# Kernel optimization log

Measured on AMD Instinct MI355X. Metric: run time of the kernel, lower is better.

## Reference

```python
import jax, jax.numpy as jnp
import numpy as np

CONF_THRES = 0.25
IOU_THRES = 0.45
MAX_DET = 300
MAX_WH = 4096.0  # class offset for class-aware (non-agnostic) NMS
B, N, NC = 16, 25200, 80


def setup_inputs() -> dict:
    key = jax.random.key(0)
    k1, k2 = jax.random.split(key)
    p = jax.random.uniform(k1, (B, N, 5 + NC), dtype=jnp.float32)
    # scale to realistic YOLO pixel-space xywh for a 640x640 image
    cx = p[..., 0] * 640.0
    cy = p[..., 1] * 640.0
    w = p[..., 2] * 96.0 + 4.0
    h = p[..., 3] * 96.0 + 4.0
    obj = p[..., 4]
    cls = p[..., 5:] * 0.9
    prediction = jnp.concatenate([jnp.stack([cx, cy, w, h, obj], axis=-1), cls], axis=-1)
    logits = jax.random.normal(k2, (B, N, NC), dtype=jnp.float32)
    return {"prediction": prediction, "logits": logits}


def xywh2xyxy(b):
    cx, cy, w, h = b[..., 0], b[..., 1], b[..., 2], b[..., 3]
    return jnp.stack([cx - w * 0.5, cy - h * 0.5, cx + w * 0.5, cy + h * 0.5], axis=-1)


def _iou_one_vs_all(box, boxes):
    # box: [4], boxes: [N,4] in xyxy
    lt = jnp.maximum(box[:2], boxes[:, :2])
    rb = jnp.minimum(box[2:], boxes[:, 2:])
    wh = jnp.clip(rb - lt, 0.0)
    inter = wh[:, 0] * wh[:, 1]
    a1 = (box[2] - box[0]) * (box[3] - box[1])
    a2 = (boxes[:, 2] - boxes[:, 0]) * (boxes[:, 3] - boxes[:, 1])
    return inter / (a1 + a2 - inter + 1e-9)


def _nms_image(x6, boxes_off, scores, log_):
    # greedy NMS, fixed MAX_DET iterations; suppressed/invalid scores are -1
    def step(s, _):
        best = jnp.argmax(s)
        keep = s[best] > 0.0
        iou = _iou_one_vs_all(boxes_off[best], boxes_off)
        s = jnp.where(iou > IOU_THRES, -1.0, s)  # also suppresses 'best' (IoU=1)
        return s, (best, keep)
    _, (idx, keep) = jax.lax.scan(step, scores, None, length=MAX_DET)
    km = keep.astype(x6.dtype)[:, None]
    dets = x6[idx] * km          # [MAX_DET, 6] zero-padded
    lg = log_[idx] * km          # [MAX_DET, 80]
    return dets, lg, keep


def reference(prediction, logits):
    obj = prediction[..., 4]                          # [B,N]
    cls_conf = prediction[..., 5:] * obj[..., None]   # x[:,5:] *= x[:,4:5]
    conf = jnp.max(cls_conf, axis=-1)                 # best class conf
    j = jnp.argmax(cls_conf, axis=-1)                 # best class index
    box = xywh2xyxy(prediction[..., :4])              # [B,N,4]
    valid = (obj > CONF_THRES) & (conf > CONF_THRES)
    scores = jnp.where(valid, conf, -1.0)
    boxes_off = box + (j.astype(box.dtype) * MAX_WH)[..., None]  # class-aware offset
    x6 = jnp.concatenate([box, conf[..., None], j.astype(box.dtype)[..., None]], axis=-1)
    dets, lg, keep = jax.vmap(_nms_image)(x6, boxes_off, scores, logits)
    return dets, lg, keep
```

## Files before the change

kernel.cpp:

```cpp
#include <hip/hip_runtime.h>
#include <cstdint>

#define BB 16
#define NN 25200
#define NCLS 80
#define ROW 85
#define MAXDET 300
#define HBINS 2048
#define CAP2 512
#define TGT 448
#define CONF_T 0.25f
#define IOU_T 0.45f
#define NT 1024

static const size_t OFF_KEYS  = 1612800;
static const size_t OFF_CBOX  = OFF_KEYS  + 65536;
static const size_t OFF_RAW   = OFF_CBOX  + 131072;
static const size_t OFF_CCLS  = OFF_RAW   + 131072;
static const size_t OFF_CCNT  = OFF_CCLS  + 32768;
static const size_t OFF_MASK  = OFF_CCNT  + 64;
static const size_t OFF_MASKT = OFF_MASK  + 524288;

__global__ __launch_bounds__(256) void k_pre(const float* __restrict__ pred,
                                             float* __restrict__ scoreArr) {
    int tid = threadIdx.x;
    int t = tid & 3;
    int row = blockIdx.x * 64 + (tid >> 2);
    const float* rp = pred + (size_t)row * ROW;
    int start = (t == 0) ? 0 : (1 + 21 * t);
    int cnt   = (t == 0) ? 22 : 21;
    float obj = rp[4];
    float best = -1.0f; int bc = 1 << 20;
#pragma unroll
    for (int k = 0; k < 22; ++k) {
        if (k < cnt) {
            int col = start + k;
            if (col >= 5) {
                float v = __fmul_rn(rp[col], obj);
                if (v > best) { best = v; bc = col; }
            }
        }
    }
#pragma unroll
    for (int d = 1; d <= 2; d <<= 1) {
        float ob = __shfl_xor(best, d);
        int   oc = __shfl_xor(bc, d);
        if (ob > best || (ob == best && oc < bc)) { best = ob; bc = oc; }
    }
    if (t == 0) {
        bool valid = (obj > CONF_T) && (best > CONF_T);
        scoreArr[row] = valid ? best : -1.0f;
    }
}

__global__ __launch_bounds__(NT) void k_sel(const float* __restrict__ pred,
                                            const float* __restrict__ scoreArr,
                                            unsigned long long* __restrict__ keysG,
                                            float4* __restrict__ cboxG,
                                            float4* __restrict__ rawG,
                                            unsigned* __restrict__ cclsG,
                                            int* __restrict__ ccnt) {
    __shared__ unsigned hist[HBINS];
    __shared__ unsigned csum[257];
    __shared__ unsigned long long keys[CAP2];
    __shared__ int flags[2];

    int b = blockIdx.x, tid = threadIdx.x;
    int lane = tid & 63;

    for (int k = tid; k < HBINS; k += NT) hist[k] = 0u;
    if (tid == 0) { flags[0] = 0; flags[1] = 0; }
    __syncthreads();

    float sreg[25];
#pragma unroll
    for (int t = 0; t < 25; ++t) {
        int n = tid + t * NT;
        float s = (n < NN) ? scoreArr[(size_t)b * NN + n] : -1.0f;
        sreg[t] = s;
        if (s > 0.0f) {
            unsigned key = (__float_as_uint(s) - 0x3E800000u) >> 13;
            if (key > HBINS - 1) key = HBINS - 1;
            atomicAdd(&hist[key], 1u);
        }
    }
    __syncthreads();

    if (tid < 256) {
        unsigned cs = 0;
#pragma unroll
        for (int t = 0; t < 8; ++t) cs += hist[tid * 8 + t];
        csum[tid] = cs;
    }
    __syncthreads();
    for (int off = 1; off < 256; off <<= 1) {
        unsigned v = 0, add = 0;
        if (tid < 256) {
            v = csum[tid];
            add = (tid + off < 256) ? csum[tid + off] : 0u;
        }
        __syncthreads();
        if (tid < 256) csum[tid] = v + add;
        __syncthreads();
    }
    if (tid < 256) {
        unsigned Sc = csum[tid];
        unsigned Sn = (tid < 255) ? csum[tid + 1] : 0u;
        if (Sc >= TGT && (tid == 255 || Sn < TGT)) {
            unsigned cum = Sn;
            int t = tid * 8;
            for (int k = tid * 8 + 7; k >= tid * 8; --k) {
                cum += hist[k];
                if (cum >= TGT) { t = k; break; }
            }
            flags[1] = t;
        }
    }
    __syncthreads();
    unsigned thr = (unsigned)flags[1];

#pragma unroll
    for (int t = 0; t < 25; ++t) {
        int n = tid + t * NT;
        float s = sreg[t];
        bool win = false;
        if (s > 0.0f) {
            unsigned key = (__float_as_uint(s) - 0x3E800000u) >> 13;
            if (key > HBINS - 1) key = HBINS - 1;
            win = (key >= thr);
        }
        unsigned long long m = __ballot(win);
        if (m) {
            int lead = __ffsll((long long)m) - 1;
            int base = 0;
            if (lane == lead) base = atomicAdd(&flags[0], __popcll(m));
            base = __shfl(base, lead);
            if (win) {
                int pos = base + __popcll(m & ((1ULL << lane) - 1ULL));
                if (pos < CAP2)
                    keys[pos] = ((unsigned long long)__float_as_uint(s) << 32)
                              | (unsigned long long)(0xFFFFFFFFu - (unsigned)n);
            }
        }
    }
    __syncthreads();
    int c = min(flags[0], CAP2);
    for (int p = tid; p < CAP2; p += NT)
        if (p >= c) keys[p] = 0ULL;
    __syncthreads();

    for (int k = 2; k <= CAP2; k <<= 1) {
        for (int j = k >> 1; j > 0; j >>= 1) {
            for (int i = tid; i < CAP2; i += NT) {
                int ixj = i ^ j;
                if (ixj > i) {
                    unsigned long long k1 = keys[i], k2 = keys[ixj];
                    bool sw = ((i & k) == 0) ? (k1 < k2) : (k1 > k2);
                    if (sw) { keys[i] = k2; keys[ixj] = k1; }
                }
            }
            __syncthreads();
        }
    }

    if (tid < CAP2) {
        int p = tid;
        if (p < c) {
            int n = (int)(0xFFFFFFFFu - (unsigned)keys[p]);
            const float* rp = pred + ((size_t)b * NN + n) * ROW;
            float cx = rp[0], cy = rp[1], w = rp[2], h = rp[3], obj = rp[4];
            float best = __fmul_rn(rp[5], obj);
            int bj = 0;
#pragma unroll 8
            for (int cc = 1; cc < NCLS; ++cc) {
                float v = __fmul_rn(rp[5 + cc], obj);
                if (v > best) { best = v; bj = cc; }
            }
            float hw = __fmul_rn(w, 0.5f), hh = __fmul_rn(h, 0.5f);
            float4 bb = make_float4(__fsub_rn(cx, hw), __fsub_rn(cy, hh),
                                    __fadd_rn(cx, hw), __fadd_rn(cy, hh));
            rawG[b * CAP2 + p] = bb;
            float off = __fmul_rn((float)bj, 4096.0f);
            cboxG[b * CAP2 + p] = make_float4(__fadd_rn(bb.x, off), __fadd_rn(bb.y, off),
                                              __fadd_rn(bb.z, off), __fadd_rn(bb.w, off));
            cclsG[b * CAP2 + p] = (unsigned)bj;
        } else {
            rawG[b * CAP2 + p]  = make_float4(0.f, 0.f, 0.f, 0.f);
            cboxG[b * CAP2 + p] = make_float4(0.f, 0.f, 0.f, 0.f);
            cclsG[b * CAP2 + p] = 0u;
        }
        keysG[b * CAP2 + p] = keys[p];
    }
    if (tid == 0) ccnt[b] = c;
}

__global__ __launch_bounds__(256) void k_mask(const float4* __restrict__ cboxG,
                                              const int* __restrict__ ccnt,
                                              unsigned long long* __restrict__ maskG,
                                              unsigned long long* __restrict__ maskTG) {
    __shared__ float4 cb[CAP2];
    int b = blockIdx.x >> 3, w = blockIdx.x & 7;
    int tid = threadIdx.x;
    cb[tid] = cboxG[b * CAP2 + tid];
    cb[256 + tid] = cboxG[b * CAP2 + 256 + tid];
    __syncthreads();
    int c = min(ccnt[b], CAP2);
    int jbase = w << 6;
    for (int i = tid; i < CAP2; i += 256) {
        unsigned long long m = 0ULL;
        if (i < c && i < jbase + 63) {
            float4 ci = cb[i];
            float a1 = __fmul_rn(__fsub_rn(ci.z, ci.x), __fsub_rn(ci.w, ci.y));
#pragma unroll 4
            for (int jj = 0; jj < 64; ++jj) {
                int j = jbase + jj;
                float4 cj = cb[j];
                float ltx = fmaxf(ci.x, cj.x), lty = fmaxf(ci.y, cj.y);
                float rbx = fminf(ci.z, cj.z), rby = fminf(ci.w, cj.w);
                float ww = fmaxf(__fsub_rn(rbx, ltx), 0.0f);
                float hh = fmaxf(__fsub_rn(rby, lty), 0.0f);
                float inter = __fmul_rn(ww, hh);
                if (j > i && inter > 0.0f) {
                    float a2 = __fmul_rn(__fsub_rn(cj.z, cj.x), __fsub_rn(cj.w, cj.y));
                    float denom = __fadd_rn(__fsub_rn(__fadd_rn(a1, a2), inter), 1e-9f);
                    if (inter / denom > IOU_T) m |= (1ULL << jj);
                }
            }
        }
        maskG[((size_t)(b * CAP2 + i)) * 8 + w] = m;
    }
    if (tid < 64) {
        int l = tid, p = jbase + l;
        unsigned long long m = 0ULL;
        if (p < c) {
            float4 cl = cb[p];
            float a2 = __fmul_rn(__fsub_rn(cl.z, cl.x), __fsub_rn(cl.w, cl.y));
            for (int ii = 0; ii < 64; ++ii) {
                float4 ci = cb[jbase + ii];
                float ltx = fmaxf(ci.x, cl.x), lty = fmaxf(ci.y, cl.y);
                float rbx = fminf(ci.z, cl.z), rby = fminf(ci.w, cl.w);
                float ww = fmaxf(__fsub_rn(rbx, ltx), 0.0f);
                float hh = fmaxf(__fsub_rn(rby, lty), 0.0f);
                float inter = __fmul_rn(ww, hh);
                if (ii < l && inter > 0.0f) {
                    float a1 = __fmul_rn(__fsub_rn(ci.z, ci.x), __fsub_rn(ci.w, ci.y));
                    float denom = __fadd_rn(__fsub_rn(__fadd_rn(a1, a2), inter), 1e-9f);
                    if (inter / denom > IOU_T) m |= (1ULL << ii);
                }
            }
        }
        maskTG[((size_t)(b * 8 + w)) * 64 + l] = m;
    }
}

__global__ __launch_bounds__(NT) void k_fin(const float* __restrict__ logits,
                                            const unsigned long long* __restrict__ keysG,
                                            const float4* __restrict__ rawG,
                                            const unsigned* __restrict__ cclsG,
                                            const int* __restrict__ ccnt,
                                            const unsigned long long* __restrict__ maskG,
                                            const unsigned long long* __restrict__ maskTG,
                                            float* __restrict__ out) {
    __shared__ unsigned long long keepm_s[8];
    __shared__ unsigned kidx[64];
    __shared__ unsigned rowsrc_s[MAXDET];
    __shared__ int s_kept;

    int b = blockIdx.x, tid = threadIdx.x;
    int c = min(ccnt[b], CAP2);

    if (tid < 64) {
        int lane = tid;
        unsigned long long remq = 0ULL;
        int kept = 0;
        for (int w = 0; w < 8; ++w) {
            int base = w << 6;
            unsigned long long tw = __shfl(remq, w);
            bool pre = ((tw >> lane) & 1ULL) != 0ULL;
            bool validl = (base + lane) < c;
            unsigned long long Cl = maskTG[((size_t)(b * 8 + w)) * 64 + lane];
            unsigned long long initK = __ballot(validl && !pre);
            unsigned long long K = initK;
            for (int it = 0; it < 64; ++it) {
                bool sup = (Cl & K & ((1ULL << lane) - 1ULL)) != 0ULL;
                unsigned long long K2 = initK & __ballot(!sup);
                if (K2 == K) break;
                K = K2;
            }
            int limit = MAXDET - kept;
            int nk = __popcll(K);
            if (nk > limit) {
                if (limit <= 0) K = 0ULL;
                else {
                    int pref = __popcll(K & ((2ULL << lane) - 1ULL));
                    bool el = ((K >> lane) & 1ULL) && (pref <= limit);
                    K = __ballot(el);
                }
            }
            kept += __popcll(K);
            if (lane == 0) keepm_s[w] = K;
            if (K != 0ULL && w < 7) {
                if ((K >> lane) & 1ULL) {
                    int r = __popcll(K & ((1ULL << lane) - 1ULL));
                    kidx[r] = (unsigned)lane;
                }
                __builtin_amdgcn_s_waitcnt(0);
                int nkk = __popcll(K);
                int q = lane & 7, slot = lane >> 3;
                unsigned long long acc = 0ULL;
                for (int t = slot; t < nkk; t += 8)
                    acc |= maskG[((size_t)(b * CAP2 + base + (int)kidx[t])) * 8 + q];
                acc |= __shfl_xor(acc, 8);
                acc |= __shfl_xor(acc, 16);
                acc |= __shfl_xor(acc, 32);
                if (slot == 0) remq |= acc;
            }
        }
        if (lane == 0) s_kept = kept;
    }
    __syncthreads();
    int kept = s_kept;

    float* dets = out;
    float* lg   = out + (size_t)BB * MAXDET * 6;
    float* kpo  = lg  + (size_t)BB * MAXDET * NCLS;

    for (int p = tid; p < CAP2; p += NT) {
        if (p < c) {
            int w = p >> 6, bitp = p & 63;
            unsigned long long kw = keepm_s[w];
            if ((kw >> bitp) & 1ULL) {
                int rank = __popcll(kw & ((1ULL << bitp) - 1ULL));
                for (int q = 0; q < w; ++q) rank += __popcll(keepm_s[q]);
                if (rank < MAXDET) {
                    float4 bb = rawG[b * CAP2 + p];
                    unsigned long long key = keysG[b * CAP2 + p];
                    float* dr = dets + ((size_t)b * MAXDET + rank) * 6;
                    dr[0] = bb.x; dr[1] = bb.y; dr[2] = bb.z; dr[3] = bb.w;
                    dr[4] = __uint_as_float((unsigned)(key >> 32));
                    dr[5] = (float)cclsG[b * CAP2 + p];
                    rowsrc_s[rank] = 0xFFFFFFFFu - (unsigned)key;
                }
            }
        }
    }
    for (int i = tid; i < MAXDET; i += NT) {
        if (i >= kept) {
            float* dr = dets + ((size_t)b * MAXDET + i) * 6;
#pragma unroll
            for (int q = 0; q < 6; ++q) dr[q] = 0.0f;
        }
        kpo[b * MAXDET + i] = (i < kept) ? 1.0f : 0.0f;
    }
    __syncthreads();
    for (int i = tid; i < MAXDET * NCLS; i += NT) {
        int t = i / NCLS, col = i - t * NCLS;
        float v = 0.0f;
        if (t < kept) v = logits[((size_t)b * NN + rowsrc_s[t]) * NCLS + col];
        lg[(size_t)b * MAXDET * NCLS + i] = v;
    }
}

extern "C" void kernel_launch(void* const* d_in, const int* in_sizes, int n_in,
                              void* d_out, int out_size, void* d_ws, size_t ws_size,
                              hipStream_t stream) {
    const float* pred   = (const float*)d_in[0];
    const float* logits = (const float*)d_in[1];
    float* out = (float*)d_out;
    char* ws = (char*)d_ws;

    float* scr = (float*)ws;
    unsigned long long* keysG  = (unsigned long long*)(ws + OFF_KEYS);
    float4* cboxG              = (float4*)(ws + OFF_CBOX);
    float4* rawG               = (float4*)(ws + OFF_RAW);
    unsigned* cclsG            = (unsigned*)(ws + OFF_CCLS);
    int* ccnt                  = (int*)(ws + OFF_CCNT);
    unsigned long long* maskG  = (unsigned long long*)(ws + OFF_MASK);
    unsigned long long* maskTG = (unsigned long long*)(ws + OFF_MASKT);

    k_pre<<<6300, 256, 0, stream>>>(pred, scr);
    k_sel<<<BB, NT, 0, stream>>>(pred, scr, keysG, cboxG, rawG, cclsG, ccnt);
    k_mask<<<BB * 8, 256, 0, stream>>>(cboxG, ccnt, maskG, maskTG);
    k_fin<<<BB, NT, 0, stream>>>(logits, keysG, rawG, cclsG, ccnt, maskG, maskTG, out);
}
```

Baseline: 346.9 us.

## Fuse histogram into pre-pass, split selection, merge mask and NMS into one kernel

Per-image score histograms are now built in k_pre with global atomics, so k_sel no longer rebuilds them. k_sel is split into 8 slices per image so compaction runs across more blocks. Sorting, box gathering, IoU mask building and greedy NMS move into a single k_fin kernel that keeps keys, boxes and masks in shared memory, which removes the separate k_mask launch and its global round trips. The cost is a memset, heavy global atomic traffic on the histogram, and a large shared-memory footprint in k_fin, where only 16 blocks do all the mask work.

New measurement: 388.0 us. +11.8%, slower.

```diff
diff --git a/kernel.cpp b/kernel.cpp
--- a/kernel.cpp
+++ b/kernel.cpp
@@ -11,18 +11,14 @@
 #define TGT 448
 #define CONF_T 0.25f
 #define IOU_T 0.45f
-#define NT 1024
-
-static const size_t OFF_KEYS  = 1612800;
-static const size_t OFF_CBOX  = OFF_KEYS  + 65536;
-static const size_t OFF_RAW   = OFF_CBOX  + 131072;
-static const size_t OFF_CCLS  = OFF_RAW   + 131072;
-static const size_t OFF_CCNT  = OFF_CCLS  + 32768;
-static const size_t OFF_MASK  = OFF_CCNT  + 64;
-static const size_t OFF_MASKT = OFF_MASK  + 524288;
+
+static const size_t OFF_CNT  = 131072;
+static const size_t OFF_KEYS = 131136;
+static const size_t OFF_SCR  = 196672;
 
 __global__ __launch_bounds__(256) void k_pre(const float* __restrict__ pred,
-                                             float* __restrict__ scoreArr) {
+                                             float* __restrict__ scoreArr,
+                                             unsigned* __restrict__ hist) {
     int tid = threadIdx.x;
     int t = tid & 3;
     int row = blockIdx.x * 64 + (tid >> 2);
@@ -50,79 +46,61 @@
     if (t == 0) {
         bool valid = (obj > CONF_T) && (best > CONF_T);
         scoreArr[row] = valid ? best : -1.0f;
+        if (valid) {
+            unsigned key = (__float_as_uint(best) - 0x3E800000u) >> 13;
+            if (key > HBINS - 1) key = HBINS - 1;
+            atomicAdd(&hist[(row / NN) * HBINS + key], 1u);
+        }
     }
 }
 
-__global__ __launch_bounds__(NT) void k_sel(const float* __restrict__ pred,
-                                            const float* __restrict__ scoreArr,
-                                            unsigned long long* __restrict__ keysG,
-                                            float4* __restrict__ cboxG,
-                                            float4* __restrict__ rawG,
-                                            unsigned* __restrict__ cclsG,
-                                            int* __restrict__ ccnt) {
-    __shared__ unsigned hist[HBINS];
+__global__ __launch_bounds__(256) void k_sel(const float* __restrict__ scoreArr,
+                                             const unsigned* __restrict__ histG,
+                                             int* __restrict__ cntG,
+                                             unsigned long long* __restrict__ keysG) {
+    __shared__ unsigned h[HBINS];
     __shared__ unsigned csum[257];
-    __shared__ unsigned long long keys[CAP2];
-    __shared__ int flags[2];
-
-    int b = blockIdx.x, tid = threadIdx.x;
-    int lane = tid & 63;
-
-    for (int k = tid; k < HBINS; k += NT) hist[k] = 0u;
-    if (tid == 0) { flags[0] = 0; flags[1] = 0; }
-    __syncthreads();
-
-    float sreg[25];
+    __shared__ int s_thr;
+    int b = blockIdx.x >> 3, slice = blockIdx.x & 7;
+    int tid = threadIdx.x, lane = tid & 63;
+
+    for (int k = tid; k < HBINS; k += 256) h[k] = histG[b * HBINS + k];
+    if (tid == 0) s_thr = 0;
+    __syncthreads();
+
+    unsigned cs = 0;
 #pragma unroll
-    for (int t = 0; t < 25; ++t) {
-        int n = tid + t * NT;
-        float s = (n < NN) ? scoreArr[(size_t)b * NN + n] : -1.0f;
-        sreg[t] = s;
-        if (s > 0.0f) {
-            unsigned key = (__float_as_uint(s) - 0x3E800000u) >> 13;
-            if (key > HBINS - 1) key = HBINS - 1;
-            atomicAdd(&hist[key], 1u);
-        }
-    }
-    __syncthreads();
-
-    if (tid < 256) {
-        unsigned cs = 0;
-#pragma unroll
-        for (int t = 0; t < 8; ++t) cs += hist[tid * 8 + t];
-        csum[tid] = cs;
-    }
+    for (int t = 0; t < 8; ++t) cs += h[tid * 8 + t];
+    csum[tid] = cs;
     __syncthreads();
     for (int off = 1; off < 256; off <<= 1) {
-        unsigned v = 0, add = 0;
-        if (tid < 256) {
-            v = csum[tid];
-            add = (tid + off < 256) ? csum[tid + off] : 0u;
-        }
+        unsigned v = csum[tid];
+        unsigned add = (tid + off < 256) ? csum[tid + off] : 0u;
         __syncthreads();
-        if (tid < 256) csum[tid] = v + add;
+        csum[tid] = v + add;
         __syncthreads();
     }
-    if (tid < 256) {
+    {
         unsigned Sc = csum[tid];
         unsigned Sn = (tid < 255) ? csum[tid + 1] : 0u;
         if (Sc >= TGT && (tid == 255 || Sn < TGT)) {
             unsigned cum = Sn;
             int t = tid * 8;
             for (int k = tid * 8 + 7; k >= tid * 8; --k) {
-                cum += hist[k];
+                cum += h[k];
                 if (cum >= TGT) { t = k; break; }
             }
-            flags[1] = t;
-        }
-    }
-    __syncthreads();
-    unsigned thr = (unsigned)flags[1];
-
-#pragma unroll
-    for (int t = 0; t < 25; ++t) {
-        int n = tid + t * NT;
-        float s = sreg[t];
+            s_thr = t;
+        }
+    }
+    __syncthreads();
+    unsigned thr = (unsigned)s_thr;
+
+    int base_n = slice * (NN / 8);
+    for (int r = 0; r < 13; ++r) {
+        int n = base_n + r * 256 + tid;
+        bool in = (r * 256 + tid) < (NN / 8);
+        float s = in ? scoreArr[(size_t)b * NN + n] : -1.0f;
         bool win = false;
         if (s > 0.0f) {
             unsigned key = (__float_as_uint(s) - 0x3E800000u) >> 13;
@@ -132,27 +110,45 @@
         unsigned long long m = __ballot(win);
         if (m) {
             int lead = __ffsll((long long)m) - 1;
-            int base = 0;
-            if (lane == lead) base = atomicAdd(&flags[0], __popcll(m));
-            base = __shfl(base, lead);
+            int basep = 0;
+            if (lane == lead) basep = atomicAdd(&cntG[b], __popcll(m));
+            basep = __shfl(basep, lead);
             if (win) {
-                int pos = base + __popcll(m & ((1ULL << lane) - 1ULL));
+                int pos = basep + __popcll(m & ((1ULL << lane) - 1ULL));
                 if (pos < CAP2)
-                    keys[pos] = ((unsigned long long)__float_as_uint(s) << 32)
-                              | (unsigned long long)(0xFFFFFFFFu - (unsigned)n);
-            }
-        }
-    }
-    __syncthreads();
-    int c = min(flags[0], CAP2);
-    for (int p = tid; p < CAP2; p += NT)
-        if (p >= c) keys[p] = 0ULL;
+                    keysG[b * CAP2 + pos] = ((unsigned long long)__float_as_uint(s) << 32)
+                                          | (unsigned long long)(0xFFFFFFFFu - (unsigned)n);
+            }
+        }
+    }
+}
+
+__global__ __launch_bounds__(1024) void k_fin(const float* __restrict__ pred,
+                                              const float* __restrict__ logits,
+                                              const unsigned long long* __restrict__ keysG,
+                                              const int* __restrict__ ccnt,
+                                              float* __restrict__ out) {
+    __shared__ unsigned long long keys[CAP2];
+    __shared__ float4 cbox[CAP2];
+    __shared__ float4 rawb[CAP2];
+    __shared__ unsigned ccls[CAP2];
+    __shared__ unsigned long long maskS[CAP2 * 8];
+    __shared__ unsigned long long maskT[8 * 64];
+    __shared__ unsigned rowsrc_s[MAXDET];
+    __shared__ unsigned kidx[64];
+    __shared__ unsigned long long keepm_s[8];
+    __shared__ int s_kept;
+
+    int b = blockIdx.x, tid = threadIdx.x;
+    int c = min(ccnt[b], CAP2);
+
+    if (tid < CAP2) keys[tid] = (tid < c) ? keysG[b * CAP2 + tid] : 0ULL;
     __syncthreads();
 
     for (int k = 2; k <= CAP2; k <<= 1) {
         for (int j = k >> 1; j > 0; j >>= 1) {
-            for (int i = tid; i < CAP2; i += NT) {
-                int ixj = i ^ j;
+            if (tid < CAP2) {
+                int i = tid, ixj = i ^ j;
                 if (ixj > i) {
                     unsigned long long k1 = keys[i], k2 = keys[ixj];
                     bool sw = ((i & k) == 0) ? (k1 < k2) : (k1 > k2);
@@ -179,42 +175,31 @@
             float hw = __fmul_rn(w, 0.5f), hh = __fmul_rn(h, 0.5f);
             float4 bb = make_float4(__fsub_rn(cx, hw), __fsub_rn(cy, hh),
                                     __fadd_rn(cx, hw), __fadd_rn(cy, hh));
-            rawG[b * CAP2 + p] = bb;
+            rawb[p] = bb;
             float off = __fmul_rn((float)bj, 4096.0f);
-            cboxG[b * CAP2 + p] = make_float4(__fadd_rn(bb.x, off), __fadd_rn(bb.y, off),
-                                              __fadd_rn(bb.z, off), __fadd_rn(bb.w, off));
-            cclsG[b * CAP2 + p] = (unsigned)bj;
+            cbox[p] = make_float4(__fadd_rn(bb.x, off), __fadd_rn(bb.y, off),
+                                  __fadd_rn(bb.z, off), __fadd_rn(bb.w, off));
+            ccls[p] = (unsigned)bj;
         } else {
-            rawG[b * CAP2 + p]  = make_float4(0.f, 0.f, 0.f, 0.f);
-            cboxG[b * CAP2 + p] = make_float4(0.f, 0.f, 0.f, 0.f);
-            cclsG[b * CAP2 + p] = 0u;
-        }
-        keysG[b * CAP2 + p] = keys[p];
-    }
-    if (tid == 0) ccnt[b] = c;
-}
-
-__global__ __launch_bounds__(256) void k_mask(const float4* __restrict__ cboxG,
-                                              const int* __restrict__ ccnt,
-                                              unsigned long long* __restrict__ maskG,
-                                              unsigned long long* __restrict__ maskTG) {
-    __shared__ float4 cb[CAP2];
-    int b = blockIdx.x >> 3, w = blockIdx.x & 7;
-    int tid = threadIdx.x;
-    cb[tid] = cboxG[b * CAP2 + tid];
-    cb[256 + tid] = cboxG[b * CAP2 + 256 + tid];
-    __syncthreads();
-    int c = min(ccnt[b], CAP2);
-    int jbase = w << 6;
-    for (int i = tid; i < CAP2; i += 256) {
+            rawb[p] = make_float4(0.f, 0.f, 0.f, 0.f);
+            cbox[p] = make_float4(0.f, 0.f, 0.f, 0.f);
+            ccls[p] = 0u;
+        }
+    }
+    __syncthreads();
+
+    for (int task = tid; task < CAP2 * 8; task += 1024) {
+        int i = task & (CAP2 - 1);
+        int w = task >> 9;
+        int jbase = w << 6;
         unsigned long long m = 0ULL;
         if (i < c && i < jbase + 63) {
-            float4 ci = cb[i];
+            float4 ci = cbox[i];
             float a1 = __fmul_rn(__fsub_rn(ci.z, ci.x), __fsub_rn(ci.w, ci.y));
 #pragma unroll 4
             for (int jj = 0; jj < 64; ++jj) {
                 int j = jbase + jj;
-                float4 cj = cb[j];
+                float4 cj = cbox[j];
                 float ltx = fmaxf(ci.x, cj.x), lty = fmaxf(ci.y, cj.y);
                 float rbx = fminf(ci.z, cj.z), rby = fminf(ci.w, cj.w);
                 float ww = fmaxf(__fsub_rn(rbx, ltx), 0.0f);
@@ -227,16 +212,17 @@
                 }
             }
         }
-        maskG[((size_t)(b * CAP2 + i)) * 8 + w] = m;
-    }
-    if (tid < 64) {
-        int l = tid, p = jbase + l;
+        maskS[i * 8 + w] = m;
+    }
+    if (tid < CAP2) {
+        int l = tid & 63, w = tid >> 6;
+        int jbase = w << 6, p = jbase + l;
         unsigned long long m = 0ULL;
         if (p < c) {
-            float4 cl = cb[p];
+            float4 cl = cbox[p];
             float a2 = __fmul_rn(__fsub_rn(cl.z, cl.x), __fsub_rn(cl.w, cl.y));
             for (int ii = 0; ii < 64; ++ii) {
-                float4 ci = cb[jbase + ii];
+                float4 ci = cbox[jbase + ii];
                 float ltx = fmaxf(ci.x, cl.x), lty = fmaxf(ci.y, cl.y);
                 float rbx = fminf(ci.z, cl.z), rby = fminf(ci.w, cl.w);
                 float ww = fmaxf(__fsub_rn(rbx, ltx), 0.0f);
@@ -249,25 +235,9 @@
                 }
             }
         }
-        maskTG[((size_t)(b * 8 + w)) * 64 + l] = m;
-    }
-}
-
-__global__ __launch_bounds__(NT) void k_fin(const float* __restrict__ logits,
-                                            const unsigned long long* __restrict__ keysG,
-                                            const float4* __restrict__ rawG,
-                                            const unsigned* __restrict__ cclsG,
-                                            const int* __restrict__ ccnt,
-                                            const unsigned long long* __restrict__ maskG,
-                                            const unsigned long long* __restrict__ maskTG,
-                                            float* __restrict__ out) {
-    __shared__ unsigned long long keepm_s[8];
-    __shared__ unsigned kidx[64];
-    __shared__ unsigned rowsrc_s[MAXDET];
-    __shared__ int s_kept;
-
-    int b = blockIdx.x, tid = threadIdx.x;
-    int c = min(ccnt[b], CAP2);
+        maskT[w * 64 + l] = m;
+    }
+    __syncthreads();
 
     if (tid < 64) {
         int lane = tid;
@@ -278,7 +248,7 @@
             unsigned long long tw = __shfl(remq, w);
             bool pre = ((tw >> lane) & 1ULL) != 0ULL;
             bool validl = (base + lane) < c;
-            unsigned long long Cl = maskTG[((size_t)(b * 8 + w)) * 64 + lane];
+            unsigned long long Cl = maskT[w * 64 + lane];
             unsigned long long initK = __ballot(validl && !pre);
             unsigned long long K = initK;
             for (int it = 0; it < 64; ++it) {
@@ -309,7 +279,7 @@
                 int q = lane & 7, slot = lane >> 3;
                 unsigned long long acc = 0ULL;
                 for (int t = slot; t < nkk; t += 8)
-                    acc |= maskG[((size_t)(b * CAP2 + base + (int)kidx[t])) * 8 + q];
+                    acc |= maskS[(base + (int)kidx[t]) * 8 + q];
                 acc |= __shfl_xor(acc, 8);
                 acc |= __shfl_xor(acc, 16);
                 acc |= __shfl_xor(acc, 32);
@@ -325,7 +295,8 @@
     float* lg   = out + (size_t)BB * MAXDET * 6;
     float* kpo  = lg  + (size_t)BB * MAXDET * NCLS;
 
-    for (int p = tid; p < CAP2; p += NT) {
+    if (tid < CAP2) {
+        int p = tid;
         if (p < c) {
             int w = p >> 6, bitp = p & 63;
             unsigned long long kw = keepm_s[w];
@@ -333,18 +304,17 @@
                 int rank = __popcll(kw & ((1ULL << bitp) - 1ULL));
                 for (int q = 0; q < w; ++q) rank += __popcll(keepm_s[q]);
                 if (rank < MAXDET) {
-                    float4 bb = rawG[b * CAP2 + p];
-                    unsigned long long key = keysG[b * CAP2 + p];
+                    float4 bb = rawb[p];
                     float* dr = dets + ((size_t)b * MAXDET + rank) * 6;
                     dr[0] = bb.x; dr[1] = bb.y; dr[2] = bb.z; dr[3] = bb.w;
-                    dr[4] = __uint_as_float((unsigned)(key >> 32));
-                    dr[5] = (float)cclsG[b * CAP2 + p];
-                    rowsrc_s[rank] = 0xFFFFFFFFu - (unsigned)key;
-                }
-            }
-        }
-    }
-    for (int i = tid; i < MAXDET; i += NT) {
+                    dr[4] = __uint_as_float((unsigned)(keys[p] >> 32));
+                    dr[5] = (float)ccls[p];
+                    rowsrc_s[rank] = 0xFFFFFFFFu - (unsigned)keys[p];
+                }
+            }
+        }
+    }
+    for (int i = tid; i < MAXDET; i += 1024) {
         if (i >= kept) {
             float* dr = dets + ((size_t)b * MAXDET + i) * 6;
 #pragma unroll
@@ -353,7 +323,7 @@
         kpo[b * MAXDET + i] = (i < kept) ? 1.0f : 0.0f;
     }
     __syncthreads();
-    for (int i = tid; i < MAXDET * NCLS; i += NT) {
+    for (int i = tid; i < MAXDET * NCLS; i += 1024) {
         int t = i / NCLS, col = i - t * NCLS;
         float v = 0.0f;
         if (t < kept) v = logits[((size_t)b * NN + rowsrc_s[t]) * NCLS + col];
@@ -369,17 +339,14 @@
     float* out = (float*)d_out;
     char* ws = (char*)d_ws;
 
-    float* scr = (float*)ws;
+    unsigned* hist             = (unsigned*)ws;
+    int* cnt                   = (int*)(ws + OFF_CNT);
     unsigned long long* keysG  = (unsigned long long*)(ws + OFF_KEYS);
-    float4* cboxG              = (float4*)(ws + OFF_CBOX);
-    float4* rawG               = (float4*)(ws + OFF_RAW);
-    unsigned* cclsG            = (unsigned*)(ws + OFF_CCLS);
-    int* ccnt                  = (int*)(ws + OFF_CCNT);
-    unsigned long long* maskG  = (unsigned long long*)(ws + OFF_MASK);
-    unsigned long long* maskTG = (unsigned long long*)(ws + OFF_MASKT);
-
-    k_pre<<<6300, 256, 0, stream>>>(pred, scr);
-    k_sel<<<BB, NT, 0, stream>>>(pred, scr, keysG, cboxG, rawG, cclsG, ccnt);
-    k_mask<<<BB * 8, 256, 0, stream>>>(cboxG, ccnt, maskG, maskTG);
-    k_fin<<<BB, NT, 0, stream>>>(logits, keysG, rawG, cclsG, ccnt, maskG, maskTG, out);
+    float* scr                 = (float*)(ws + OFF_SCR);
+
+    hipMemsetAsync(ws, 0, OFF_KEYS, stream);
+
+    k_pre<<<6300, 256, 0, stream>>>(pred, scr, hist);
+    k_sel<<<BB * 8, 256, 0, stream>>>(scr, hist, cnt, keysG);
+    k_fin<<<BB, 1024, 0, stream>>>(pred, logits, keysG, cnt, out);
 }
```
